# Optimization experiments

Measured on AMD Instinct MI355X. Metric: run time of the kernel, lower is better.

Reference implementation:

```python
import jax, jax.numpy as jnp
import numpy as np

LEBESGUE_P = 3          # lebesgue_p from __init__
WEIGHT_RANGE = 0.1      # weight init scale
B, C_IN, H, W = 32, 96, 56, 56
C_OUT, K = 384, 3
STRIDE = (1, 1)
PADDING = ((1, 1), (1, 1))


def setup_inputs() -> dict:
    key = jax.random.key(0)
    kx, kw = jax.random.split(key)
    x = jax.random.normal(kx, (B, C_IN, H, W), dtype=jnp.float32)
    # learned buffer 'weight': [out_channels, in_channels, kH, kW]
    weight = jax.random.normal(kw, (C_OUT, C_IN, K, K), dtype=jnp.float32) * WEIGHT_RANGE
    return {"x": x, "weight": weight}


def reference(x, weight):
    # get_pre_activations: conv with power-transformed weight sign(w)*|w|^(p-1)
    w_eff = jnp.sign(weight) * jnp.abs(weight) ** (LEBESGUE_P - 1)
    pre_x = jax.lax.conv_general_dilated(
        x, w_eff,
        window_strides=STRIDE,
        padding=PADDING,
        dimension_numbers=("NCHW", "OIHW", "NCHW"),
    )  # [B, C_OUT, H, W]

    # get_wta (groups=1): hard winner-take-all over channel dim per (b, h, w).
    # Original transposes/reshapes to [C_OUT, B*H*W], argmax over dim 0, one_hot,
    # then reshapes back; mathematically identical to a channel-axis argmax+one_hot.
    winners = jnp.argmax(pre_x, axis=1)                                   # [B, H, W]
    wta = jax.nn.one_hot(winners, pre_x.shape[1], axis=1, dtype=pre_x.dtype)  # [B, C_OUT, H, W]

    # forward(x, return_x_wta=True) returns (pre_x, wta); stack so output is one array
    return jnp.stack([pre_x, wta], axis=0)  # [2, B, C_OUT, H, W]
```

## Files before the change

### kernel.cpp

```cpp
#include <hip/hip_runtime.h>
#include <math.h>
#include <stdint.h>

#define CIN  96
#define COUT 384
#define HH   56
#define WW   56
#define BB   32

#define MARGIN   2e-3f
#define CAP      32000u
#define WT32_OFF (256 * 1024)
#define WT64_OFF (2 * 1024 * 1024)
#define WT16_OFF (5 * 1024 * 1024)
#define POSB     8

#define HL2      331776
#define XSB      6336

typedef _Float16 half8 __attribute__((ext_vector_type(8)));
typedef float    f32x4 __attribute__((ext_vector_type(4)));

template <bool WITH16>
__global__ void prep_weights(const float* __restrict__ w, float* __restrict__ wt32,
                             double* __restrict__ wt64, _Float16* __restrict__ wt16,
                             uint32_t* __restrict__ cnt) {
    int idx = blockIdx.x * blockDim.x + threadIdx.x;
    if (idx == 0) *cnt = 0u;
    if (idx >= COUT * CIN * 9) return;
    int co = idx / (CIN * 9);
    int r  = idx - co * (CIN * 9);
    double d = (double)w[idx];
    double e = d * fabs(d);
    wt64[(size_t)r * COUT + co] = e;
    float ef = (float)e;
    wt32[(size_t)r * COUT + co] = ef;
    if (WITH16) {
        _Float16 hi = (_Float16)ef;
        _Float16 lo = (_Float16)(ef - (float)hi);
        int ci  = r / 9;
        int khw = r - ci * 9;
        int off = (((co >> 4) * 12 + (ci >> 3)) * 9 + khw) * 128 + (co & 15) * 8 + (ci & 7);
        wt16[off] = hi;
        wt16[off + HL2] = lo;
    }
}

__global__ __launch_bounds__(512, 4)
void conv_mfma(const float* __restrict__ x, const _Float16* __restrict__ wt16,
               float* __restrict__ out, uint32_t* __restrict__ cnt,
               uint32_t* __restrict__ flags) {
    const int h   = blockIdx.x;
    const int b   = blockIdx.y;
    const int tid = threadIdx.x;
    const int l   = tid & 63;
    const int wg  = tid >> 6;
    const int g   = l >> 4;
    const int c   = l & 15;

    __shared__ char lds[33792];
    _Float16* xs  = (_Float16*)lds;
    float*    T   = (float*)lds;
    float4*   red = (float4*)(lds + 25344);
    int*      win = (int*)(lds + 25344 + 8192);

    f32x4 acc[4][3];
    #pragma unroll
    for (int mf = 0; mf < 4; ++mf)
        #pragma unroll
        for (int nf = 0; nf < 3; ++nf)
            #pragma unroll
            for (int q = 0; q < 4; ++q) acc[mf][nf][q] = 0.0f;

    const _Float16* pa0 = xs + (g * 198 + c) * 8;

    auto stage = [&](int chunk) {
        _Float16* xsb = xs + (chunk & 1) * XSB;
        const int ci0 = chunk * 32;
        for (int idx = tid; idx < 4 * 198; idx += 512) {
            int cq  = idx / 198;
            int rem = idx - cq * 198;
            int r   = rem / 66;
            int col = rem - r * 66;
            int gh  = h + r - 1;
            int gw  = col - 1;
            half8 hv = {};
            if ((unsigned)gh < 56u && (unsigned)gw < 56u) {
                const float* px = x + (((size_t)b * CIN + (ci0 + cq * 8)) * HH + gh) * WW + gw;
                #pragma unroll
                for (int i = 0; i < 8; ++i) hv[i] = (_Float16)px[i * 3136];
            }
            *(half8*)(xsb + (size_t)(cq * 198 + rem) * 8) = hv;
        }
    };

    stage(0);
    __syncthreads();

    for (int chunk = 0; chunk < 3; ++chunk) {
        if (chunk < 2) stage(chunk + 1);

        const _Float16* pax = pa0 + (chunk & 1) * XSB;
        const _Float16* pb0 = wt16 + (size_t)(((wg * 3 + 0) * 12 + chunk * 4 + g) * 9) * 128 + c * 8;
        const _Float16* pb1 = wt16 + (size_t)(((wg * 3 + 1) * 12 + chunk * 4 + g) * 9) * 128 + c * 8;
        const _Float16* pb2 = wt16 + (size_t)(((wg * 3 + 2) * 12 + chunk * 4 + g) * 9) * 128 + c * 8;

        half8 B0 = *(const half8*)(pb0);
        half8 B1 = *(const half8*)(pb1);
        half8 B2 = *(const half8*)(pb2);

        #pragma unroll
        for (int khw = 0; khw < 9; ++khw) {
            const int kh = khw / 3;
            const int kw = khw - kh * 3;
            half8 Bn0, Bn1, Bn2;
            if (khw < 8) {
                Bn0 = *(const half8*)(pb0 + (khw + 1) * 128);
                Bn1 = *(const half8*)(pb1 + (khw + 1) * 128);
                Bn2 = *(const half8*)(pb2 + (khw + 1) * 128);
            }
            #pragma unroll
            for (int mf = 0; mf < 4; ++mf) {
                half8 Ah = *(const half8*)(pax + (kh * 66 + mf * 16 + kw) * 8);
                acc[mf][0] = __builtin_amdgcn_mfma_f32_16x16x32_f16(Ah, B0, acc[mf][0], 0, 0, 0);
                acc[mf][1] = __builtin_amdgcn_mfma_f32_16x16x32_f16(Ah, B1, acc[mf][1], 0, 0, 0);
                acc[mf][2] = __builtin_amdgcn_mfma_f32_16x16x32_f16(Ah, B2, acc[mf][2], 0, 0, 0);
            }
            if (khw < 8) { B0 = Bn0; B1 = Bn1; B2 = Bn2; }
        }
        __syncthreads();
    }

    #pragma unroll
    for (int mf = 0; mf < 4; ++mf) {
        #pragma unroll
        for (int q = 0; q < 4; ++q) {
            float best = acc[mf][0][q];
            int   bco  = wg * 48 + c;
            float sec  = -1e30f;
            #pragma unroll
            for (int nf = 1; nf < 3; ++nf) {
                float v = acc[mf][nf][q];
                if (v > best) { sec = best; best = v; bco = wg * 48 + nf * 16 + c; }
                else if (v > sec) sec = v;
            }
            #pragma unroll
            for (int off = 1; off <= 8; off <<= 1) {
                float ov = __shfl_xor(best, off, 64);
                int   oc = __shfl_xor(bco,  off, 64);
                float os = __shfl_xor(sec,  off, 64);
                if (ov > best || (ov == best && oc < bco)) {
                    sec = fmaxf(best, os);
                    best = ov; bco = oc;
                } else {
                    sec = fmaxf(sec, ov);
                }
            }
            if (c == 0) {
                int m = mf * 16 + g * 4 + q;
                red[wg * 64 + m] = make_float4(best, sec, __int_as_float(bco), 0.0f);
            }
        }
    }
    __syncthreads();
    {
        const int m = tid >> 3;
        const int j = tid & 7;
        float4 v = red[j * 64 + m];
        float best = v.x, sec = v.y;
        int   bco  = __float_as_int(v.z);
        #pragma unroll
        for (int off = 1; off <= 4; off <<= 1) {
            float ov = __shfl_xor(best, off, 64);
            int   oc = __shfl_xor(bco,  off, 64);
            float os = __shfl_xor(sec,  off, 64);
            if (ov > best || (ov == best && oc < bco)) {
                sec = fmaxf(best, os);
                best = ov; bco = oc;
            } else {
                sec = fmaxf(sec, ov);
            }
        }
        if (j == 0 && m < 56) {
            win[m] = bco;
            if ((best - sec) < MARGIN) {
                uint32_t k = atomicAdd(cnt, 1u);
                if (k < CAP) flags[k] = (uint32_t)((b * 56 + h) * 56 + m);
            }
        }
    }
    __syncthreads();

    const size_t wta_off = (size_t)BB * COUT * HH * WW;
    for (int rnd = 0; rnd < 4; ++rnd) {
        if ((wg >> 1) == rnd) {
            const int wq = wg & 1;
            #pragma unroll
            for (int mf = 0; mf < 4; ++mf)
                #pragma unroll
                for (int nf = 0; nf < 3; ++nf)
                    #pragma unroll
                    for (int q = 0; q < 4; ++q)
                        T[(wq * 48 + nf * 16 + c) * 65 + mf * 16 + g * 4 + q] = acc[mf][nf][q];
        }
        __syncthreads();
        for (int t = tid; t < 96 * 64; t += 512) {
            int co_l = t >> 6;
            int m    = t & 63;
            if (m < 56) {
                int co  = rnd * 96 + co_l;
                float v = T[co_l * 65 + m];
                size_t o = ((size_t)(b * COUT + co)) * 3136 + (size_t)h * 56 + m;
                out[o] = v;
                out[wta_off + o] = (co == win[m]) ? 1.0f : 0.0f;
            }
        }
        __syncthreads();
    }
}

__global__ __launch_bounds__(512, 2)
void conv_wta_f32(const float* __restrict__ x, const float* __restrict__ wt,
                  float* __restrict__ out, uint32_t* __restrict__ cnt,
                  uint32_t* __restrict__ flags) {
    const int h0  = blockIdx.x * 2;
    const int b   = blockIdx.y;
    const int tid = threadIdx.x;
    const int cg  = tid & 63;
    const int wg  = tid >> 6;
    const int co0 = cg * 6;
    const int ws0 = wg * 7;

    __shared__ float xs[32 * 4 * 58];
    __shared__ int   win[2][56];

    float acc[2][6][7];
    #pragma unroll
    for (int r = 0; r < 2; ++r)
        #pragma unroll
        for (int c = 0; c < 6; ++c)
            #pragma unroll
            for (int i = 0; i < 7; ++i) acc[r][c][i] = 0.0f;

    for (int chunk = 0; chunk < 3; ++chunk) {
        const int ci0 = chunk * 32;
        __syncthreads();
        for (int idx = tid; idx < 32 * 4 * 58; idx += 512) {
            int ci  = idx / 232;
            int rem = idx - ci * 232;
            int r   = rem / 58;
            int c   = rem - r * 58;
            int gh  = h0 + r - 1;
            int gw  = c - 1;
            float v = 0.0f;
            if ((unsigned)gh < 56u && (unsigned)gw < 56u)
                v = x[(((size_t)b * CIN + (ci0 + ci)) * HH + gh) * WW + gw];
            xs[idx] = v;
        }
        __syncthreads();
        for (int ci = 0; ci < 32; ++ci) {
            const int gci = ci0 + ci;
            #pragma unroll
            for (int kh = 0; kh < 3; ++kh) {
                float xa[9], xb[9];
                const float* xr0 = &xs[(ci * 4 + kh) * 58 + ws0];
                const float* xr1 = &xs[(ci * 4 + kh + 1) * 58 + ws0];
                #pragma unroll
                for (int j = 0; j < 9; ++j) { xa[j] = xr0[j]; xb[j] = xr1[j]; }
                #pragma unroll
                for (int kw = 0; kw < 3; ++kw) {
                    const float* p = wt + (size_t)((gci * 3 + kh) * 3 + kw) * COUT + co0;
                    float2 w01 = *(const float2*)(p);
                    float2 w23 = *(const float2*)(p + 2);
                    float2 w45 = *(const float2*)(p + 4);
                    float wd[6] = {w01.x, w01.y, w23.x, w23.y, w45.x, w45.y};
                    #pragma unroll
                    for (int c = 0; c < 6; ++c)
                        #pragma unroll
                        for (int i = 0; i < 7; ++i) {
                            acc[0][c][i] = fmaf(wd[c], xa[i + kw], acc[0][c][i]);
                            acc[1][c][i] = fmaf(wd[c], xb[i + kw], acc[1][c][i]);
                        }
                }
            }
        }
    }

    #pragma unroll
    for (int rr = 0; rr < 2; ++rr) {
        #pragma unroll
        for (int i = 0; i < 7; ++i) {
            float best = acc[rr][0][i];
            int   bco  = co0;
            float sec  = -1e30f;
            #pragma unroll
            for (int c = 1; c < 6; ++c) {
                float v = acc[rr][c][i];
                if (v > best) { sec = best; best = v; bco = co0 + c; }
                else if (v > sec) sec = v;
            }
            #pragma unroll
            for (int off = 32; off > 0; off >>= 1) {
                float ov = __shfl_xor(best, off, 64);
                int   oc = __shfl_xor(bco,  off, 64);
                float os = __shfl_xor(sec,  off, 64);
                if (ov > best || (ov == best && oc < bco)) {
                    sec = fmaxf(best, os);
                    best = ov; bco = oc;
                } else {
                    sec = fmaxf(sec, ov);
                }
            }
            if (cg == 0) {
                win[rr][ws0 + i] = bco;
                if ((best - sec) < MARGIN) {
                    uint32_t k = atomicAdd(cnt, 1u);
                    if (k < CAP) flags[k] = (uint32_t)((b * 56 + (h0 + rr)) * 56 + (ws0 + i));
                }
            }
        }
    }

    const size_t wta_off = (size_t)BB * COUT * HH * WW;
    float* ldsT = xs;
    __syncthreads();
    for (int k = 0; k < 8; ++k) {
        if ((cg >> 3) == k) {
            const int cr = (cg & 7) * 6;
            #pragma unroll
            for (int c = 0; c < 6; ++c)
                #pragma unroll
                for (int rr = 0; rr < 2; ++rr)
                    #pragma unroll
                    for (int i = 0; i < 7; ++i)
                        ldsT[(cr + c) * 113 + rr * 56 + ws0 + i] = acc[rr][c][i];
        }
        __syncthreads();
        for (int l = tid; l < 48 * 112; l += 512) {
            int co_r = l / 112;
            int rem  = l - co_r * 112;
            int rr   = rem / 56;
            int w    = rem - rr * 56;
            int co   = k * 48 + co_r;
            float v  = ldsT[co_r * 113 + rem];
            size_t o = ((size_t)(b * COUT + co)) * 3136 + (size_t)(h0 + rr) * 56 + w;
            out[o] = v;
            out[wta_off + o] = (co == win[rr][w]) ? 1.0f : 0.0f;
        }
        __syncthreads();
    }
}

__global__ __launch_bounds__(384)
void fixup_f64(const float* __restrict__ x, const double* __restrict__ wt64,
               float* __restrict__ out, const uint32_t* __restrict__ cnt,
               const uint32_t* __restrict__ flags) {
    __shared__ float  xp[POSB][CIN * 9];
    __shared__ double sv[POSB][COUT];
    __shared__ int winners[POSB];

    uint32_t n = *cnt;
    if (n > CAP) n = CAP;
    const int tid = threadIdx.x;
    const int wg  = tid >> 6;
    const int lane = tid & 63;
    const size_t wta_off = (size_t)BB * COUT * HH * WW;

    for (uint32_t base = blockIdx.x * POSB; base < n; base += gridDim.x * POSB) {
        int np = (int)(n - base) < POSB ? (int)(n - base) : POSB;
        __syncthreads();
        for (int idx = tid; idx < np * CIN * 9; idx += 384) {
            int p  = idx / (CIN * 9);
            int r  = idx - p * (CIN * 9);
            int ci = r / 9;
            int k  = r - ci * 9;
            int kh = k / 3, kw = k - kh * 3;
            uint32_t pos = flags[base + p];
            int w_ = pos % 56;
            int h_ = (pos / 56) % 56;
            int b_ = pos / 3136;
            int gh = h_ + kh - 1, gw = w_ + kw - 1;
            float v = 0.0f;
            if ((unsigned)gh < 56u && (unsigned)gw < 56u)
                v = x[(((size_t)b_ * CIN + ci) * HH + gh) * WW + gw];
            xp[p][r] = v;
        }
        __syncthreads();
        {
            const int co = tid;
            double a[POSB];
            #pragma unroll
            for (int p = 0; p < POSB; ++p) a[p] = 0.0;
            #pragma unroll 4
            for (int r = 0; r < CIN * 9; ++r) {
                double wd = wt64[(size_t)r * COUT + co];
                #pragma unroll
                for (int p = 0; p < POSB; ++p)
                    a[p] = fma(wd, (double)xp[p][r], a[p]);
            }
            #pragma unroll
            for (int p = 0; p < POSB; ++p) sv[p][co] = a[p];
        }
        __syncthreads();
        for (int p = wg; p < np; p += 6) {
            double best = sv[p][lane * 6];
            int bco = lane * 6;
            #pragma unroll
            for (int c = 1; c < 6; ++c) {
                double v2 = sv[p][lane * 6 + c];
                if (v2 > best) { best = v2; bco = lane * 6 + c; }
            }
            #pragma unroll
            for (int off = 32; off > 0; off >>= 1) {
                double ov = __shfl_xor(best, off, 64);
                int    oc = __shfl_xor(bco,  off, 64);
                if (ov > best || (ov == best && oc < bco)) { best = ov; bco = oc; }
            }
            if (lane == 0) winners[p] = bco;
        }
        __syncthreads();
        for (int idx = tid; idx < np * COUT; idx += 384) {
            int p  = idx / COUT;
            int co = idx - p * COUT;
            uint32_t pos = flags[base + p];
            int w_ = pos % 56;
            int h_ = (pos / 56) % 56;
            int b_ = pos / 3136;
            size_t o = (((size_t)b_ * COUT + co) * HH + h_) * WW + w_;
            out[o] = (float)sv[p][co];
            out[wta_off + o] = (co == winners[p]) ? 1.0f : 0.0f;
        }
        __syncthreads();
    }
}

__global__ __launch_bounds__(256, 2)
void conv_wta_f64(const float* __restrict__ x, const float* __restrict__ wraw,
                  float* __restrict__ out) {
    const int whalf = blockIdx.x;
    const int h     = blockIdx.y;
    const int b     = blockIdx.z;
    const int tid   = threadIdx.x;
    const int cg    = tid & 63;
    const int wg    = tid >> 6;
    const int co0   = cg * 6;
    const int wbase = whalf * 28 + wg * 7;

    __shared__ float xs[32 * 3 * 30];
    double acc[6][7];
    #pragma unroll
    for (int c = 0; c < 6; ++c)
        #pragma unroll
        for (int i = 0; i < 7; ++i) acc[c][i] = 0.0;

    for (int chunk = 0; chunk < 3; ++chunk) {
        const int ci0 = chunk * 32;
        __syncthreads();
        for (int idx = tid; idx < 32 * 3 * 30; idx += 256) {
            int ci = idx / 90, rem = idx - ci * 90;
            int r = rem / 30, c = rem - r * 30;
            int gh = h + r - 1, gw = whalf * 28 - 1 + c;
            float v = 0.0f;
            if ((unsigned)gh < 56u && (unsigned)gw < 56u)
                v = x[(((size_t)b * CIN + (ci0 + ci)) * HH + gh) * WW + gw];
            xs[idx] = v;
        }
        __syncthreads();
        for (int ci = 0; ci < 32; ++ci) {
            const int gci = ci0 + ci;
            #pragma unroll
            for (int kh = 0; kh < 3; ++kh) {
                double xd[9];
                #pragma unroll
                for (int j = 0; j < 9; ++j)
                    xd[j] = (double)xs[(ci * 3 + kh) * 30 + wg * 7 + j];
                #pragma unroll
                for (int kw = 0; kw < 3; ++kw) {
                    #pragma unroll
                    for (int c = 0; c < 6; ++c) {
                        double d = (double)wraw[(size_t)(co0 + c) * (CIN * 9) + gci * 9 + kh * 3 + kw];
                        double wd = d * fabs(d);
                        #pragma unroll
                        for (int i = 0; i < 7; ++i)
                            acc[c][i] = fma(wd, xd[i + kw], acc[c][i]);
                    }
                }
            }
        }
    }
    const size_t wta_off = (size_t)BB * COUT * HH * WW;
    #pragma unroll
    for (int i = 0; i < 7; ++i) {
        double best = acc[0][i];
        int bco = co0;
        #pragma unroll
        for (int c = 1; c < 6; ++c)
            if (acc[c][i] > best) { best = acc[c][i]; bco = co0 + c; }
        #pragma unroll
        for (int off = 32; off > 0; off >>= 1) {
            double ov = __shfl_xor(best, off, 64);
            int    oc = __shfl_xor(bco,  off, 64);
            if (ov > best || (ov == best && oc < bco)) { best = ov; bco = oc; }
        }
        const int w = wbase + i;
        #pragma unroll
        for (int c = 0; c < 6; ++c) {
            size_t o = (((size_t)b * COUT + (co0 + c)) * HH + h) * WW + w;
            out[o] = (float)acc[c][i];
            out[wta_off + o] = (co0 + c == bco) ? 1.0f : 0.0f;
        }
    }
}

extern "C" void kernel_launch(void* const* d_in, const int* in_sizes, int n_in,
                              void* d_out, int out_size, void* d_ws, size_t ws_size,
                              hipStream_t stream) {
    (void)in_sizes; (void)n_in; (void)out_size;
    const float* x = (const float*)d_in[0];
    const float* w = (const float*)d_in[1];
    float* out = (float*)d_out;

    const size_t need16 = (size_t)WT16_OFF + (size_t)2 * HL2 * sizeof(_Float16);
    const size_t need64 = (size_t)WT64_OFF + (size_t)COUT * CIN * 9 * sizeof(double);

    uint32_t* cnt   = (uint32_t*)d_ws;
    uint32_t* flags = (uint32_t*)((char*)d_ws + 256);
    float*    wt32  = (float*)((char*)d_ws + WT32_OFF);
    double*   wt64  = (double*)((char*)d_ws + WT64_OFF);
    _Float16* wt16  = (_Float16*)((char*)d_ws + WT16_OFF);

    if (ws_size >= need16) {
        prep_weights<true><<<(COUT * CIN * 9 + 255) / 256, 256, 0, stream>>>(w, wt32, wt64, wt16, cnt);
        conv_mfma<<<dim3(56, 32), 512, 0, stream>>>(x, wt16, out, cnt, flags);
        fixup_f64<<<256, 384, 0, stream>>>(x, wt64, out, cnt, flags);
    } else if (ws_size >= need64) {
        prep_weights<false><<<(COUT * CIN * 9 + 255) / 256, 256, 0, stream>>>(w, wt32, wt64, wt16, cnt);
        conv_wta_f32<<<dim3(28, 32), 512, 0, stream>>>(x, wt32, out, cnt, flags);
        fixup_f64<<<256, 384, 0, stream>>>(x, wt64, out, cnt, flags);
    } else {
        conv_wta_f64<<<dim3(2, 56, 32), 256, 0, stream>>>(x, w, out);
    }
}
```

Measured before the change: 332.2 us.

## Process two output rows per conv_mfma block to raise weight reuse

Each conv_mfma block now computes two output rows (112 pixels as 7 M-fragments) instead of one, halving the grid and sharing each loaded weight fragment across more MFMAs. The staged input tile grows to four padded rows, and the reduction, winner and store phases are reworked for 112 positions, with per-wave store rounds. prep_weights is also changed to write coalesced along output channels. More accumulators raise register pressure, so launch bounds drop to 3 waves' occupancy, and the grid has fewer blocks to spread across CUs.

```diff
diff --git a/kernel.cpp b/kernel.cpp
--- a/kernel.cpp
+++ b/kernel.cpp
@@ -16,7 +16,7 @@
 #define POSB     8
 
 #define HL2      331776
-#define XSB      6336
+#define XSB2     8448
 
 typedef _Float16 half8 __attribute__((ext_vector_type(8)));
 typedef float    f32x4 __attribute__((ext_vector_type(4)));
@@ -28,9 +28,9 @@
     int idx = blockIdx.x * blockDim.x + threadIdx.x;
     if (idx == 0) *cnt = 0u;
     if (idx >= COUT * CIN * 9) return;
-    int co = idx / (CIN * 9);
-    int r  = idx - co * (CIN * 9);
-    double d = (double)w[idx];
+    int r  = idx / COUT;
+    int co = idx - r * COUT;
+    double d = (double)w[(size_t)co * (CIN * 9) + r];
     double e = d * fabs(d);
     wt64[(size_t)r * COUT + co] = e;
     float ef = (float)e;
@@ -46,11 +46,11 @@
     }
 }
 
-__global__ __launch_bounds__(512, 4)
+__global__ __launch_bounds__(512, 3)
 void conv_mfma(const float* __restrict__ x, const _Float16* __restrict__ wt16,
                float* __restrict__ out, uint32_t* __restrict__ cnt,
                uint32_t* __restrict__ flags) {
-    const int h   = blockIdx.x;
+    const int h0  = blockIdx.x * 2;
     const int b   = blockIdx.y;
     const int tid = threadIdx.x;
     const int l   = tid & 63;
@@ -58,31 +58,38 @@
     const int g   = l >> 4;
     const int c   = l & 15;
 
-    __shared__ char lds[33792];
+    __shared__ char lds[34240];
     _Float16* xs  = (_Float16*)lds;
     float*    T   = (float*)lds;
-    float4*   red = (float4*)(lds + 25344);
-    int*      win = (int*)(lds + 25344 + 8192);
-
-    f32x4 acc[4][3];
-    #pragma unroll
-    for (int mf = 0; mf < 4; ++mf)
+    float4*   red = (float4*)lds;
+    int*      win = (int*)(lds + 33792);
+
+    f32x4 acc[7][3];
+    #pragma unroll
+    for (int mf = 0; mf < 7; ++mf)
         #pragma unroll
         for (int nf = 0; nf < 3; ++nf)
             #pragma unroll
             for (int q = 0; q < 4; ++q) acc[mf][nf][q] = 0.0f;
 
-    const _Float16* pa0 = xs + (g * 198 + c) * 8;
+    int base_m[7];
+    #pragma unroll
+    for (int mf = 0; mf < 7; ++mf) {
+        int m  = mf * 16 + c;
+        int r0 = (m >= 56) ? 1 : 0;
+        int col = m - 56 * r0;
+        base_m[mf] = (g * 4 + r0) * 66 + col;
+    }
 
     auto stage = [&](int chunk) {
-        _Float16* xsb = xs + (chunk & 1) * XSB;
+        _Float16* xsb = xs + (chunk & 1) * XSB2;
         const int ci0 = chunk * 32;
-        for (int idx = tid; idx < 4 * 198; idx += 512) {
-            int cq  = idx / 198;
-            int rem = idx - cq * 198;
+        for (int idx = tid; idx < 4 * 264; idx += 512) {
+            int cq  = idx / 264;
+            int rem = idx - cq * 264;
             int r   = rem / 66;
             int col = rem - r * 66;
-            int gh  = h + r - 1;
+            int gh  = h0 + r - 1;
             int gw  = col - 1;
             half8 hv = {};
             if ((unsigned)gh < 56u && (unsigned)gw < 56u) {
@@ -90,7 +97,7 @@
                 #pragma unroll
                 for (int i = 0; i < 8; ++i) hv[i] = (_Float16)px[i * 3136];
             }
-            *(half8*)(xsb + (size_t)(cq * 198 + rem) * 8) = hv;
+            *(half8*)(xsb + (size_t)idx * 8) = hv;
         }
     };
 
@@ -100,7 +107,7 @@
     for (int chunk = 0; chunk < 3; ++chunk) {
         if (chunk < 2) stage(chunk + 1);
 
-        const _Float16* pax = pa0 + (chunk & 1) * XSB;
+        const _Float16* xc  = xs + (chunk & 1) * XSB2;
         const _Float16* pb0 = wt16 + (size_t)(((wg * 3 + 0) * 12 + chunk * 4 + g) * 9) * 128 + c * 8;
         const _Float16* pb1 = wt16 + (size_t)(((wg * 3 + 1) * 12 + chunk * 4 + g) * 9) * 128 + c * 8;
         const _Float16* pb2 = wt16 + (size_t)(((wg * 3 + 2) * 12 + chunk * 4 + g) * 9) * 128 + c * 8;
@@ -120,8 +127,8 @@
                 Bn2 = *(const half8*)(pb2 + (khw + 1) * 128);
             }
             #pragma unroll
-            for (int mf = 0; mf < 4; ++mf) {
-                half8 Ah = *(const half8*)(pax + (kh * 66 + mf * 16 + kw) * 8);
+            for (int mf = 0; mf < 7; ++mf) {
+                half8 Ah = *(const half8*)(xc + (size_t)(base_m[mf] + kh * 66 + kw) * 8);
                 acc[mf][0] = __builtin_amdgcn_mfma_f32_16x16x32_f16(Ah, B0, acc[mf][0], 0, 0, 0);
                 acc[mf][1] = __builtin_amdgcn_mfma_f32_16x16x32_f16(Ah, B1, acc[mf][1], 0, 0, 0);
                 acc[mf][2] = __builtin_amdgcn_mfma_f32_16x16x32_f16(Ah, B2, acc[mf][2], 0, 0, 0);
@@ -132,7 +139,7 @@
     }
 
     #pragma unroll
-    for (int mf = 0; mf < 4; ++mf) {
+    for (int mf = 0; mf < 7; ++mf) {
         #pragma unroll
         for (int q = 0; q < 4; ++q) {
             float best = acc[mf][0][q];
@@ -158,59 +165,71 @@
             }
             if (c == 0) {
                 int m = mf * 16 + g * 4 + q;
-                red[wg * 64 + m] = make_float4(best, sec, __int_as_float(bco), 0.0f);
+                red[wg * 112 + m] = make_float4(best, sec, __int_as_float(bco), 0.0f);
             }
         }
     }
     __syncthreads();
     {
-        const int m = tid >> 3;
-        const int j = tid & 7;
-        float4 v = red[j * 64 + m];
-        float best = v.x, sec = v.y;
-        int   bco  = __float_as_int(v.z);
-        #pragma unroll
-        for (int off = 1; off <= 4; off <<= 1) {
-            float ov = __shfl_xor(best, off, 64);
-            int   oc = __shfl_xor(bco,  off, 64);
-            float os = __shfl_xor(sec,  off, 64);
-            if (ov > best || (ov == best && oc < bco)) {
-                sec = fmaxf(best, os);
-                best = ov; bco = oc;
+        const int m = tid >> 2;
+        const int j = tid & 3;
+        if (m < 112) {
+            float4 a = red[j * 112 + m];
+            float4 d = red[(j + 4) * 112 + m];
+            float best = a.x, sec = a.y;
+            int   bco  = __float_as_int(a.z);
+            if (d.x > best || (d.x == best && __float_as_int(d.z) < bco)) {
+                sec = fmaxf(best, d.y);
+                best = d.x; bco = __float_as_int(d.z);
             } else {
-                sec = fmaxf(sec, ov);
-            }
-        }
-        if (j == 0 && m < 56) {
-            win[m] = bco;
-            if ((best - sec) < MARGIN) {
-                uint32_t k = atomicAdd(cnt, 1u);
-                if (k < CAP) flags[k] = (uint32_t)((b * 56 + h) * 56 + m);
+                sec = fmaxf(sec, d.x);
+            }
+            #pragma unroll
+            for (int off = 1; off <= 2; off <<= 1) {
+                float ov = __shfl_xor(best, off, 64);
+                int   oc = __shfl_xor(bco,  off, 64);
+                float os = __shfl_xor(sec,  off, 64);
+                if (ov > best || (ov == best && oc < bco)) {
+                    sec = fmaxf(best, os);
+                    best = ov; bco = oc;
+                } else {
+                    sec = fmaxf(sec, ov);
+                }
+            }
+            if (j == 0) {
+                win[m] = bco;
+                if ((best - sec) < MARGIN) {
+                    int rr = (m >= 56) ? 1 : 0;
+                    int w  = m - 56 * rr;
+                    uint32_t k = atomicAdd(cnt, 1u);
+                    if (k < CAP) flags[k] = (uint32_t)((b * 56 + h0 + rr) * 56 + w);
+                }
             }
         }
     }
     __syncthreads();
 
     const size_t wta_off = (size_t)BB * COUT * HH * WW;
-    for (int rnd = 0; rnd < 4; ++rnd) {
-        if ((wg >> 1) == rnd) {
-            const int wq = wg & 1;
-            #pragma unroll
-            for (int mf = 0; mf < 4; ++mf)
+    for (int rnd = 0; rnd < 8; ++rnd) {
+        if (wg == rnd) {
+            #pragma unroll
+            for (int mf = 0; mf < 7; ++mf)
                 #pragma unroll
                 for (int nf = 0; nf < 3; ++nf)
                     #pragma unroll
                     for (int q = 0; q < 4; ++q)
-                        T[(wq * 48 + nf * 16 + c) * 65 + mf * 16 + g * 4 + q] = acc[mf][nf][q];
-        }
-        __syncthreads();
-        for (int t = tid; t < 96 * 64; t += 512) {
-            int co_l = t >> 6;
-            int m    = t & 63;
-            if (m < 56) {
-                int co  = rnd * 96 + co_l;
-                float v = T[co_l * 65 + m];
-                size_t o = ((size_t)(b * COUT + co)) * 3136 + (size_t)h * 56 + m;
+                        T[(nf * 16 + c) * 113 + mf * 16 + g * 4 + q] = acc[mf][nf][q];
+        }
+        __syncthreads();
+        for (int t = tid; t < 48 * 128; t += 512) {
+            int co_l = t >> 7;
+            int m    = t & 127;
+            if (m < 112) {
+                int co  = rnd * 48 + co_l;
+                int rr  = (m >= 56) ? 1 : 0;
+                int w   = m - 56 * rr;
+                float v = T[co_l * 113 + m];
+                size_t o = ((size_t)(b * COUT + co)) * 3136 + (size_t)(h0 + rr) * 56 + w;
                 out[o] = v;
                 out[wta_off + o] = (co == win[m]) ? 1.0f : 0.0f;
             }
@@ -531,7 +550,7 @@
 
     if (ws_size >= need16) {
         prep_weights<true><<<(COUT * CIN * 9 + 255) / 256, 256, 0, stream>>>(w, wt32, wt64, wt16, cnt);
-        conv_mfma<<<dim3(56, 32), 512, 0, stream>>>(x, wt16, out, cnt, flags);
+        conv_mfma<<<dim3(28, 32), 512, 0, stream>>>(x, wt16, out, cnt, flags);
         fixup_f64<<<256, 384, 0, stream>>>(x, wt64, out, cnt, flags);
     } else if (ws_size >= need64) {
         prep_weights<false><<<(COUT * CIN * 9 + 255) / 256, 256, 0, stream>>>(w, wt32, wt64, wt16, cnt);
```

Measured after the change: 362.2 us. 9.0% more time.
